# Kernel optimization log

Measured on AMD Instinct MI355X. Metric: run time of the kernel, lower is better.

The kernel has to match this reference:

```python
import jax, jax.numpy as jnp
import numpy as np

GDEP = 2
ALPHA = 0.5
C_OUT = 128   # = N (node dim)
NODE_DIM = 40
B, C, L = 32, 64, 64
LN_EPS = 1e-5


def setup_inputs() -> dict:
    key = jax.random.key(0)
    ks = jax.random.split(key, 7)
    x = jax.random.normal(ks[0], (B, C_OUT, C, L), dtype=jnp.float32)
    nodevec1 = jax.random.normal(ks[1], (C_OUT, NODE_DIM), dtype=jnp.float32)
    nodevec2 = jax.random.normal(ks[2], (NODE_DIM, C_OUT), dtype=jnp.float32)
    k_in = (GDEP + 1) * C_OUT
    conv_w = jax.random.normal(ks[3], (C_OUT, k_in), dtype=jnp.float32) * (1.0 / np.sqrt(k_in))
    conv_b = jax.random.normal(ks[4], (C_OUT,), dtype=jnp.float32) * 0.02
    ln_w = jnp.ones((C_OUT,), dtype=jnp.float32)
    ln_b = jnp.zeros((C_OUT,), dtype=jnp.float32)
    return {"x": x, "nodevec1": nodevec1, "nodevec2": nodevec2,
            "conv_w": conv_w, "conv_b": conv_b, "ln_w": ln_w, "ln_b": ln_b}


def reference(x, nodevec1, nodevec2, conv_w, conv_b, ln_w, ln_b):
    # adaptive adjacency: (N, N)
    adp = jax.nn.softmax(jax.nn.relu(nodevec1 @ nodevec2), axis=1)
    # mixprop: add self loops, row-normalize
    adj = adp + jnp.eye(adp.shape[0], dtype=adp.dtype)
    a = adj / adj.sum(axis=1, keepdims=True)  # (N, N)
    h = x
    outs = [h]
    for _ in range(GDEP):
        # nconv: out[b,v,c,l] = sum_w a[v,w] * h[b,w,c,l]
        h = ALPHA * x + (1.0 - ALPHA) * jnp.einsum('bwcl,vw->bvcl', h, a)
        outs.append(h)
    ho = jnp.concatenate(outs, axis=1)  # (B, (GDEP+1)*N, C, L)
    # 1x1 conv over channel dim
    ho = jnp.einsum('bkcl,ok->bocl', ho, conv_w) + conv_b[None, :, None, None]
    out = jax.nn.gelu(ho, approximate=False)  # torch nn.GELU default is exact erf
    b, n = x.shape[0], x.shape[1]
    y = (x + out).reshape(b, n, -1).transpose(0, 2, 1)  # (B, C*L, N)
    mean = y.mean(axis=-1, keepdims=True)
    var = jnp.mean(jnp.square(y - mean), axis=-1, keepdims=True)
    return (y - mean) * jax.lax.rsqrt(var + LN_EPS) * ln_w + ln_b
```

## Files before the change

### kernel.cpp

```cpp
#include <hip/hip_runtime.h>
#include <hip/hip_bf16.h>
#include <math.h>

#define NN 128
#define ND 40
#define BB 32
#define CC 64
#define LL 64
#define GDIM (CC*LL)

typedef __attribute__((ext_vector_type(8))) short bf16x8;
typedef __attribute__((ext_vector_type(16))) float f32x16;

static __device__ __forceinline__ unsigned pk2(float a, float b) {
    __hip_bfloat162 h;
    h.x = __float2bfloat16(a);
    h.y = __float2bfloat16(b);
    return *(unsigned*)&h;
}
static __device__ __forceinline__ float bl(unsigned u) { return __uint_as_float(u << 16); }
static __device__ __forceinline__ float bh(unsigned u) { return __uint_as_float(u & 0xffff0000u); }

static __device__ __forceinline__ float gelu(float v) {
    float v2 = v * v;
    float zn = v * fmaf(v2, -0.07135481627f, -1.5957691216f);
    float e  = __expf(zn);
    return v * __builtin_amdgcn_rcpf(1.f + e);
}

__global__ __launch_bounds__(128) void k_adj(const float* __restrict__ nv1,
                                             const float* __restrict__ nv2,
                                             float* __restrict__ A) {
    int t = threadIdx.x;
    int r = blockIdx.x * 2 + (t >> 6);
    int l = t & 63;
    float s0 = 0.f, s1 = 0.f;
#pragma unroll
    for (int k = 0; k < ND; ++k) {
        float a = nv1[r * ND + k];
        s0 = fmaf(a, nv2[k * NN + l], s0);
        s1 = fmaf(a, nv2[k * NN + 64 + l], s1);
    }
    s0 = fmaxf(s0, 0.f);
    s1 = fmaxf(s1, 0.f);
    float m = fmaxf(s0, s1);
#pragma unroll
    for (int d = 32; d; d >>= 1) m = fmaxf(m, __shfl_xor(m, d));
    float e0 = expf(s0 - m), e1 = expf(s1 - m);
    float ss = e0 + e1;
#pragma unroll
    for (int d = 32; d; d >>= 1) ss += __shfl_xor(ss, d);
    float p0 = e0 / ss, p1 = e1 / ss;
    float ps = p0 + p1;
#pragma unroll
    for (int d = 32; d; d >>= 1) ps += __shfl_xor(ps, d);
    float ra = 1.f / (ps + 1.f);
    A[r * NN + l]      = (p0 + (l == r ? 1.f : 0.f)) * ra;
    A[r * NN + 64 + l] = (p1 + ((l + 64) == r ? 1.f : 0.f)) * ra;
}

__global__ __launch_bounds__(256) void k_mm(const float* __restrict__ A,
                                            const float* __restrict__ W,
                                            short* __restrict__ Mfrag) {
    __shared__ float Al[NN * 132];
    __shared__ float red[256];
    __shared__ float cl[NN];
    const int t = threadIdx.x;
    const int o = blockIdx.x;

    {
        const float4* As = (const float4*)A;
#pragma unroll
        for (int q = 0; q < 16; ++q) {
            int i = t + q * 256;
            int r = i >> 5, c4 = (i & 31) * 4;
            *(float4*)(Al + r * 132 + c4) = As[i];
        }
    }
    __syncthreads();

    const int u = t & 127, h = t >> 7;

    float tp = 0.f;
    const float* w2p = W + o * 384 + 256 + h * 64;
#pragma unroll 8
    for (int w2 = 0; w2 < 64; ++w2)
        tp = fmaf(w2p[w2], Al[(h * 64 + w2) * 132 + u], tp);
    red[t] = tp;
    __syncthreads();
    if (t < NN) {
        float tt = red[t] + red[t + 128];
        cl[t] = fmaf(0.25f, tt, fmaf(0.5f, W[o * 384 + 128 + t],
                                     0.25f * W[o * 384 + 256 + t]));
    }
    __syncthreads();

    float mp = 0.f;
#pragma unroll 8
    for (int w2 = 0; w2 < 64; ++w2)
        mp = fmaf(cl[h * 64 + w2], Al[(h * 64 + w2) * 132 + u], mp);
    red[t] = mp;
    __syncthreads();
    if (t < NN) {
        float m = W[o * 384 + t] + 0.5f * (W[o * 384 + 128 + t] + W[o * 384 + 256 + t])
                + red[t] + red[t + 128];
        int kk = t >> 4, hi2 = (t >> 3) & 1, e = t & 7;
        int ti = (o >> 5) * 64 + hi2 * 32 + (o & 31);
        __hip_bfloat16 hb = __float2bfloat16(m);
        Mfrag[kk * 2048 + ti * 8 + e] = *(short*)&hb;
    }
}

__global__ __launch_bounds__(256, 5) void k_main(const float* __restrict__ x,
                                                 const short* __restrict__ Mfrag,
                                                 const float* __restrict__ cb,
                                                 const float* __restrict__ lnw,
                                                 const float* __restrict__ lnb,
                                                 float* __restrict__ out) {
    __shared__ short xsT[LL * NN];
    __shared__ float cbs[NN], lnws[NN], lnbs[NN];
    __shared__ float mu[LL], rsg[LL];

    const int t = threadIdx.x;
    const int c = blockIdx.x, b = blockIdx.y;
    const int w = t >> 6, l = t & 63;

    bf16x8 af[8];
#pragma unroll
    for (int kk = 0; kk < 8; ++kk)
        af[kk] = *(const bf16x8*)(Mfrag + kk * 2048 + t * 8);

    const float* xsrc = x + (size_t)b * NN * GDIM + (size_t)c * LL;
    char* xbb = (char*)xsT;
#pragma unroll
    for (int q = 0; q < 2; ++q) {
        int j = t + q * 256;
        int pq = j & 15, vq = j >> 4;
        int pb = pq * 4;
        const float* rp = xsrc + (size_t)(vq * 4) * GDIM + pb;
        float4 r0 = *(const float4*)(rp);
        float4 r1 = *(const float4*)(rp + GDIM);
        float4 r2 = *(const float4*)(rp + 2 * GDIM);
        float4 r3 = *(const float4*)(rp + 3 * GDIM);
        float c0[4] = {r0.x, r0.y, r0.z, r0.w};
        float c1[4] = {r1.x, r1.y, r1.z, r1.w};
        float c2[4] = {r2.x, r2.y, r2.z, r2.w};
        float c3[4] = {r3.x, r3.y, r3.z, r3.w};
#pragma unroll
        for (int jj = 0; jj < 4; ++jj) {
            int p = pb + jj;
            uint2 wv;
            wv.x = pk2(c0[jj], c1[jj]);
            wv.y = pk2(c2[jj], c3[jj]);
            *(uint2*)(xbb + p * 256 + ((vq * 8) ^ ((p & 15) << 4))) = wv;
        }
    }
    if (t < NN) { cbs[t] = cb[t]; lnws[t] = lnw[t]; lnbs[t] = lnb[t]; }
    __syncthreads();

    const int hi = l >> 5;
    const int pc0 = l & 31, pc1 = 32 + (l & 31);
    const int sw = (l & 15) << 4;
    const char* xrb = (const char*)xsT;

    f32x16 acc0, acc1;
#pragma unroll
    for (int i = 0; i < 16; ++i) { acc0[i] = 0.f; acc1[i] = 0.f; }

#pragma unroll
    for (int kk = 0; kk < 8; ++kk) {
        int kb = kk * 32 + hi * 16;
        bf16x8 b0 = *(const bf16x8*)(xrb + pc0 * 256 + (kb ^ sw));
        bf16x8 b1 = *(const bf16x8*)(xrb + pc1 * 256 + (kb ^ sw));
        acc0 = __builtin_amdgcn_mfma_f32_32x32x16_bf16(af[kk], b0, acc0, 0, 0, 0);
        acc1 = __builtin_amdgcn_mfma_f32_32x32x16_bf16(af[kk], b1, acc1, 0, 0, 0);
    }
    __syncthreads();

    const int vh = hi * 4;
    char* ywb = (char*)xsT;
#pragma unroll
    for (int g = 0; g < 4; ++g) {
        const int vb = w * 32 + g * 8 + vh;
        const float cb0 = cbs[vb], cb1 = cbs[vb + 1], cb2 = cbs[vb + 2], cb3 = cbs[vb + 3];
        {
            char* sp = ywb + pc0 * 256 + ((vb * 2) ^ sw);
            uint2 xw = *(const uint2*)sp;
            float y0 = bl(xw.x) + gelu(acc0[4 * g + 0] + cb0);
            float y1 = bh(xw.x) + gelu(acc0[4 * g + 1] + cb1);
            float y2 = bl(xw.y) + gelu(acc0[4 * g + 2] + cb2);
            float y3 = bh(xw.y) + gelu(acc0[4 * g + 3] + cb3);
            uint2 yw; yw.x = pk2(y0, y1); yw.y = pk2(y2, y3);
            *(uint2*)sp = yw;
        }
        {
            char* sp = ywb + pc1 * 256 + ((vb * 2) ^ sw);
            uint2 xw = *(const uint2*)sp;
            float y0 = bl(xw.x) + gelu(acc1[4 * g + 0] + cb0);
            float y1 = bh(xw.x) + gelu(acc1[4 * g + 1] + cb1);
            float y2 = bl(xw.y) + gelu(acc1[4 * g + 2] + cb2);
            float y3 = bh(xw.y) + gelu(acc1[4 * g + 3] + cb3);
            uint2 yw; yw.x = pk2(y0, y1); yw.y = pk2(y2, y3);
            *(uint2*)sp = yw;
        }
    }
    __syncthreads();

    {
        int p = w * 16 + (l >> 2), sub = l & 3;
        int mask = (p & 15) << 4;
        const char* base = xrb + p * 256;
        float s = 0.f, s2 = 0.f;
#pragma unroll
        for (int j = 0; j < 8; ++j) {
            uint2 u = *(const uint2*)(base + ((sub * 64 + j * 8) ^ mask));
            float a0 = bl(u.x), a1 = bh(u.x), a2 = bl(u.y), a3 = bh(u.y);
            s += (a0 + a1) + (a2 + a3);
            s2 = fmaf(a0, a0, fmaf(a1, a1, fmaf(a2, a2, fmaf(a3, a3, s2))));
        }
        s  += __shfl_xor(s, 1);  s  += __shfl_xor(s, 2);
        s2 += __shfl_xor(s2, 1); s2 += __shfl_xor(s2, 2);
        if (sub == 0) {
            float mean = s * (1.f / NN);
            float var  = s2 * (1.f / NN) - mean * mean;
            mu[p]  = mean;
            rsg[p] = rsqrtf(var + 1e-5f);
        }
    }
    __syncthreads();

    {
        float* op = out + ((size_t)b * GDIM + (size_t)c * LL) * NN;
#pragma unroll
        for (int kk = 0; kk < 8; ++kk) {
            int i = t + kk * 256;
            int p = i >> 5, v4 = (i & 31) * 4;
            int mask = (p & 15) << 4;
            uint2 u = *(const uint2*)(xrb + p * 256 + ((v4 * 2) ^ mask));
            float4 lw = *(const float4*)(lnws + v4);
            float4 lb = *(const float4*)(lnbs + v4);
            float mm = mu[p], rr = rsg[p];
            float4 o4;
            o4.x = (bl(u.x) - mm) * rr * lw.x + lb.x;
            o4.y = (bh(u.x) - mm) * rr * lw.y + lb.y;
            o4.z = (bl(u.y) - mm) * rr * lw.z + lb.z;
            o4.w = (bh(u.y) - mm) * rr * lw.w + lb.w;
            *(float4*)(op + p * NN + v4) = o4;
        }
    }
}

extern "C" void kernel_launch(void* const* d_in, const int* in_sizes, int n_in,
                              void* d_out, int out_size, void* d_ws, size_t ws_size,
                              hipStream_t stream) {
    const float* x   = (const float*)d_in[0];
    const float* nv1 = (const float*)d_in[1];
    const float* nv2 = (const float*)d_in[2];
    const float* cw  = (const float*)d_in[3];
    const float* cb  = (const float*)d_in[4];
    const float* lnw = (const float*)d_in[5];
    const float* lnb = (const float*)d_in[6];
    float* out = (float*)d_out;

    short* Mfrag = (short*)d_ws;
    float* A     = (float*)((char*)d_ws + 32768);

    k_adj<<<64, 128, 0, stream>>>(nv1, nv2, A);
    k_mm <<<NN, 256, 0, stream>>>(A, cw, Mfrag);
    k_main<<<dim3(CC, BB), 256, 0, stream>>>(x, Mfrag, cb, lnw, lnb, out);
}
```

Measured before the change: 38.20 us.

## Fuse LayerNorm statistics into GELU epilogue and raise occupancy bound

Per-position sum and sum-of-squares are now accumulated in registers while the GELU epilogue produces y. They are reduced across the two half-waves with a shuffle and across the four waves through a small shared array, which removes a separate pass that re-read the bf16 tile from LDS. Statistics now come from fp32 values instead of the rounded bf16 ones, so results shift slightly. The launch-bounds occupancy hint goes from 5 to 7 blocks per CU, which may cap registers and cause spills.

```diff
diff --git a/kernel.cpp b/kernel.cpp
--- a/kernel.cpp
+++ b/kernel.cpp
@@ -111,7 +111,7 @@
     }
 }
 
-__global__ __launch_bounds__(256, 5) void k_main(const float* __restrict__ x,
+__global__ __launch_bounds__(256, 7) void k_main(const float* __restrict__ x,
                                                  const short* __restrict__ Mfrag,
                                                  const float* __restrict__ cb,
                                                  const float* __restrict__ lnw,
@@ -120,6 +120,7 @@
     __shared__ short xsT[LL * NN];
     __shared__ float cbs[NN], lnws[NN], lnbs[NN];
     __shared__ float mu[LL], rsg[LL];
+    __shared__ float psum[4][LL], psq[4][LL];
 
     const int t = threadIdx.x;
     const int c = blockIdx.x, b = blockIdx.y;
@@ -179,6 +180,7 @@
 
     const int vh = hi * 4;
     char* ywb = (char*)xsT;
+    float sA = 0.f, qA = 0.f, sB = 0.f, qB = 0.f;
 #pragma unroll
     for (int g = 0; g < 4; ++g) {
         const int vb = w * 32 + g * 8 + vh;
@@ -190,6 +192,8 @@
             float y1 = bh(xw.x) + gelu(acc0[4 * g + 1] + cb1);
             float y2 = bl(xw.y) + gelu(acc0[4 * g + 2] + cb2);
             float y3 = bh(xw.y) + gelu(acc0[4 * g + 3] + cb3);
+            sA += (y0 + y1) + (y2 + y3);
+            qA = fmaf(y0, y0, fmaf(y1, y1, fmaf(y2, y2, fmaf(y3, y3, qA))));
             uint2 yw; yw.x = pk2(y0, y1); yw.y = pk2(y2, y3);
             *(uint2*)sp = yw;
         }
@@ -200,32 +204,27 @@
             float y1 = bh(xw.x) + gelu(acc1[4 * g + 1] + cb1);
             float y2 = bl(xw.y) + gelu(acc1[4 * g + 2] + cb2);
             float y3 = bh(xw.y) + gelu(acc1[4 * g + 3] + cb3);
+            sB += (y0 + y1) + (y2 + y3);
+            qB = fmaf(y0, y0, fmaf(y1, y1, fmaf(y2, y2, fmaf(y3, y3, qB))));
             uint2 yw; yw.x = pk2(y0, y1); yw.y = pk2(y2, y3);
             *(uint2*)sp = yw;
         }
     }
-    __syncthreads();
-
-    {
-        int p = w * 16 + (l >> 2), sub = l & 3;
-        int mask = (p & 15) << 4;
-        const char* base = xrb + p * 256;
-        float s = 0.f, s2 = 0.f;
-#pragma unroll
-        for (int j = 0; j < 8; ++j) {
-            uint2 u = *(const uint2*)(base + ((sub * 64 + j * 8) ^ mask));
-            float a0 = bl(u.x), a1 = bh(u.x), a2 = bl(u.y), a3 = bh(u.y);
-            s += (a0 + a1) + (a2 + a3);
-            s2 = fmaf(a0, a0, fmaf(a1, a1, fmaf(a2, a2, fmaf(a3, a3, s2))));
-        }
-        s  += __shfl_xor(s, 1);  s  += __shfl_xor(s, 2);
-        s2 += __shfl_xor(s2, 1); s2 += __shfl_xor(s2, 2);
-        if (sub == 0) {
-            float mean = s * (1.f / NN);
-            float var  = s2 * (1.f / NN) - mean * mean;
-            mu[p]  = mean;
-            rsg[p] = rsqrtf(var + 1e-5f);
-        }
+    sA += __shfl_xor(sA, 32); qA += __shfl_xor(qA, 32);
+    sB += __shfl_xor(sB, 32); qB += __shfl_xor(qB, 32);
+    if (hi == 0) {
+        psum[w][pc0] = sA; psq[w][pc0] = qA;
+        psum[w][pc1] = sB; psq[w][pc1] = qB;
+    }
+    __syncthreads();
+
+    if (t < LL) {
+        float s = (psum[0][t] + psum[1][t]) + (psum[2][t] + psum[3][t]);
+        float q = (psq[0][t]  + psq[1][t])  + (psq[2][t]  + psq[3][t]);
+        float mean = s * (1.f / NN);
+        float var  = q * (1.f / NN) - mean * mean;
+        mu[t]  = mean;
+        rsg[t] = rsqrtf(var + 1e-5f);
     }
     __syncthreads();
 
```

Measured after the change: 38.96 us. About the same (+2.0%).
